# Optimization experiments

Hardware: AMD Instinct MI355X
Metric: run time of the kernel (lower is better)

The kernel has to match this reference:

```python
import jax, jax.numpy as jnp
import numpy as np

B, S, D = 4, 2048, 1024
N_NEURONS, K = 512, 8
N_BASIS, R = 32, 512
N_HEADS = 8
D_HEAD = R // N_HEADS


def setup_inputs() -> dict:
    key = jax.random.key(0)
    ks = jax.random.split(key, 8)
    x = jax.random.normal(ks[0], (B, S, D), dtype=jnp.float32)
    W_router = jax.random.normal(ks[1], (N_NEURONS, D), dtype=jnp.float32) / np.sqrt(D)
    recipe_Q = jax.random.normal(ks[2], (N_NEURONS, N_BASIS), dtype=jnp.float32)
    recipe_K = jax.random.normal(ks[3], (N_NEURONS, N_BASIS), dtype=jnp.float32)
    recipe_V = jax.random.normal(ks[4], (N_NEURONS, N_BASIS), dtype=jnp.float32)
    # orthonormal basis: QR of random [D, R] per basis slot (buffer, not trained)
    raw = jax.random.normal(ks[5], (N_BASIS, D, R), dtype=jnp.float32)
    basis = jax.vmap(lambda m: jnp.linalg.qr(m)[0])(raw)  # [N_BASIS, D, R]
    W_o = jax.random.normal(ks[6], (D, R), dtype=jnp.float32) / np.sqrt(R)
    mask = jnp.tril(jnp.ones((S, S), dtype=jnp.int32))[None, None]  # [1,1,S,S] causal
    mask = jnp.broadcast_to(mask, (B, 1, S, S))
    return {"x": x, "W_router": W_router, "recipe_Q": recipe_Q, "recipe_K": recipe_K,
            "recipe_V": recipe_V, "basis": basis, "W_o": W_o, "mask": mask}


def reference(x, W_router, recipe_Q, recipe_K, recipe_V, basis, W_o, mask):
    # routing: pick top-k neurons per token
    scores = jnp.einsum('bsd,nd->bsn', x, W_router)            # [B,S,N_NEURONS]
    topk_scores, topk_idx = jax.lax.top_k(scores, K)            # [B,S,K]
    weights = jax.nn.softmax(topk_scores, axis=-1)              # [B,S,K]

    def token_recipe(recipe):
        g = recipe[topk_idx]                                    # [B,S,K,N_BASIS]
        r = jnp.einsum('bskn,bsk->bsn', g, weights)             # [B,S,N_BASIS]
        return jax.nn.softmax(r, axis=-1)

    tQ = token_recipe(recipe_Q)
    tK = token_recipe(recipe_K)
    tV = token_recipe(recipe_V)

    # shared basis projection of x, reused for Q/K/V (same math as
    # W = einsum('bsn,ndr->bsdr'); Q = einsum('bsd,bsdr->bsr'))
    P = jnp.einsum('bsd,ndr->bsnr', x, basis)                   # [B,S,N_BASIS,R]
    Q = jnp.einsum('bsnr,bsn->bsr', P, tQ)
    Kt = jnp.einsum('bsnr,bsn->bsr', P, tK)
    V = jnp.einsum('bsnr,bsn->bsr', P, tV)

    def heads(t):
        return t.reshape(B, S, N_HEADS, D_HEAD).transpose(0, 2, 1, 3)  # [B,H,S,dh]

    Qh, Kh, Vh = heads(Q), heads(Kt), heads(V)
    attn = jnp.einsum('bhqd,bhkd->bhqk', Qh, Kh) / np.sqrt(D_HEAD)
    attn = jnp.where(mask == 0, jnp.float32(-1e30), attn)
    attn = jax.nn.softmax(attn, axis=-1)                        # dropout p: eval/no-op
    out = jnp.einsum('bhqk,bhkd->bhqd', attn, Vh)
    out = out.transpose(0, 2, 1, 3).reshape(B, S, R)
    attn_out = jnp.einsum('bsr,dr->bsd', out, W_o)
    return attn_out, topk_idx, weights
```

## Files before the change

kernel.cpp:

```cpp
#include <hip/hip_runtime.h>
#include <math.h>
#include <stdint.h>


typedef __attribute__((ext_vector_type(4))) float f32x4;
typedef __attribute__((ext_vector_type(8))) short s16x8;
typedef __attribute__((ext_vector_type(4))) short s16x4;
typedef __attribute__((ext_vector_type(4))) int i32x4;
typedef __attribute__((ext_vector_type(8))) int i32x8;

#define DEV __device__ __forceinline__

DEV short f2bf(float f){
  union { float f; unsigned u; } c; c.f = f;
  unsigned u = c.u;
  unsigned r = (u + 0x7fffu + ((u >> 16) & 1u)) >> 16;
  return (short)r;
}
DEV float bf2f(short s){
  union { unsigned u; float f; } c; c.u = ((unsigned)(unsigned short)s) << 16;
  return c.f;
}
DEV unsigned char f2e4m3(float f){
  union { float f; unsigned u; } c; c.f = f;
  unsigned u = c.u;
  unsigned sign = (u >> 24) & 0x80u;
  unsigned a = u & 0x7fffffffu;
  if (a >= 0x43e00000u) return (unsigned char)(sign | 0x7Eu);
  if (a < 0x3c800000u){
    union { unsigned u; float f; } d; d.u = a;
    int q = (int)(d.f * 512.0f + 0.5f);
    return (unsigned char)(sign | (unsigned)q);
  }
  unsigned m = a & 0x7fffffu;
  unsigned e = (a >> 23) - 120u;
  unsigned keep = m >> 20;
  unsigned rest = m & 0xFFFFFu;
  if (rest > 0x80000u || (rest == 0x80000u && (keep & 1u))){
    keep++;
    if (keep == 8u){ keep = 0; e++; }
  }
  if (e >= 16u || (e == 15u && keep == 7u)) return (unsigned char)(sign | 0x7Eu);
  return (unsigned char)(sign | (e << 3) | keep);
}

typedef __attribute__((address_space(3))) void lds_vt;
typedef const __attribute__((address_space(1))) void g_vt;
DEV void gload16(const void* g, void* lds){
  __builtin_amdgcn_global_load_lds((g_vt*)g, (lds_vt*)lds, 16, 0, 0);
}

DEV int gslot(int c){ return (c < 4) ? (c << 1) : (((c - 4) << 1) + 1); }

__global__ void k_conv_w(const float* __restrict__ Wo, const float* __restrict__ Wrt,
                         short* __restrict__ Wob, short* __restrict__ Wrtb){
  int i = blockIdx.x*256 + threadIdx.x;
  const float* src = (i < 131072) ? Wo : Wrt;
  short* dst = (i < 131072) ? Wob : Wrtb;
  int j = (i < 131072) ? i : (i - 131072);
  float4 v = ((const float4*)src)[j];
  s16x4 o; o[0]=f2bf(v.x); o[1]=f2bf(v.y); o[2]=f2bf(v.z); o[3]=f2bf(v.w);
  ((s16x4*)dst)[j] = o;
}

__global__ void k_conv_x(const float* __restrict__ in, short* __restrict__ Xb, char* __restrict__ Xf8){
  int t = blockIdx.x*256 + threadIdx.x;
  size_t d = (size_t)t * 16;
  const float4* s = (const float4*)(in + d);
  float vals[16];
  #pragma unroll
  for (int q=0;q<4;q++){ float4 v = s[q]; vals[q*4]=v.x; vals[q*4+1]=v.y; vals[q*4+2]=v.z; vals[q*4+3]=v.w; }
  s16x8 ob0, ob1;
  unsigned long long v0 = 0, v1 = 0;
  #pragma unroll
  for (int e=0;e<8;e++){
    ob0[e] = f2bf(vals[e]);
    ob1[e] = f2bf(vals[8+e]);
    v0 |= ((unsigned long long)f2e4m3(vals[e]))   << (8*e);
    v1 |= ((unsigned long long)f2e4m3(vals[8+e])) << (8*e);
  }
  *(s16x8*)(Xb + d) = ob0;
  *(s16x8*)(Xb + d + 8) = ob1;
  int c = t & 7;
  char* dst = Xf8 + (d & ~(size_t)127) + (gslot(c) << 4);
  *(unsigned long long*)dst = v0;
  *(unsigned long long*)(dst + 8) = v1;
}

__global__ __launch_bounds__(256) void k_conv_basis8(const float* __restrict__ basis, char* __restrict__ B2f){
  __shared__ float tile[64][65];
  int tid = threadIdx.x;
  int r0 = blockIdx.x<<6, d0 = blockIdx.y<<6, n = blockIdx.z;
  const float* src = basis + ((size_t)n*1024 + d0)*512 + r0;
  for (int i = tid; i < 4096; i += 256){ int dd = i>>6, rr = i&63; tile[dd][rr] = src[(size_t)dd*512 + rr]; }
  __syncthreads();
  int rr = tid >> 2, j = tid & 3;
  unsigned long long v0 = 0, v1 = 0;
  #pragma unroll
  for (int e=0;e<8;e++){
    v0 |= ((unsigned long long)f2e4m3(tile[j*16+e][rr]))   << (8*e);
    v1 |= ((unsigned long long)f2e4m3(tile[j*16+8+e][rr])) << (8*e);
  }
  int c = j + ((d0 >> 4) & 4);
  char* dst = B2f + ((size_t)(r0+rr)*32 + n)*1024 + (size_t)(d0 & ~127) + (gslot(c) << 4);
  *(unsigned long long*)dst = v0;
  *(unsigned long long*)(dst + 8) = v1;
}

__global__ __launch_bounds__(256) void k_gemm_c32(
    const short* __restrict__ A, const short* __restrict__ Bt, int Kd, int Mblk,
    float* __restrict__ C, int ldc)
{
  __shared__ char smem[32768];
  short* Asm = (short*)smem;
  short* Bsm = (short*)(smem + 16384);
  int tid = threadIdx.x, lane = tid & 63, w = tid >> 6;
  int wr = w >> 1, wc = w & 1;
  int nwg = gridDim.x, bid = blockIdx.x;
  int sid = (bid & 7) * (nwg >> 3) + (bid >> 3);
  int row0 = (sid % Mblk) << 7;
  int col0 = (sid / Mblk) << 7;
  f32x4 acc[4][4];
  #pragma unroll
  for (int m=0;m<4;m++)
    #pragma unroll
    for (int nf=0;nf<4;nf++)
      #pragma unroll
      for (int e=0;e<4;e++) acc[m][nf][e] = 0.f;
  int lr8 = lane >> 3;
  int lk_sw = (((lane & 7) ^ (lane >> 3)) << 3);
  for (int k0 = 0; k0 < Kd; k0 += 64){
    #pragma unroll
    for (int i=0;i<4;i++){
      int chunk = (w<<2) + i;
      int r = (chunk<<3) + lr8;
      gload16(A  + (size_t)(row0 + r)*Kd + k0 + lk_sw, smem + chunk*1024);
      gload16(Bt + (size_t)(col0 + r)*Kd + k0 + lk_sw, smem + 16384 + chunk*1024);
    }
    __syncthreads();
    #pragma unroll
    for (int kk=0; kk<2; kk++){
      int csw = (kk*32 + ((lane>>4)<<3)) ^ ((lane & 7) << 3);
      s16x8 af[4], bfr[4];
      #pragma unroll
      for (int m=0;m<4;m++)
        af[m] = *(const s16x8*)(Asm + ((wr*64 + m*16 + (lane&15))*64 + csw));
      #pragma unroll
      for (int nf=0;nf<4;nf++)
        bfr[nf] = *(const s16x8*)(Bsm + ((wc*64 + nf*16 + (lane&15))*64 + csw));
      #pragma unroll
      for (int m=0;m<4;m++)
        #pragma unroll
        for (int nf=0;nf<4;nf++)
          acc[m][nf] = __builtin_amdgcn_mfma_f32_16x16x32_bf16(af[m], bfr[nf], acc[m][nf], 0, 0, 0);
    }
    __syncthreads();
  }
  #pragma unroll
  for (int m=0;m<4;m++)
    #pragma unroll
    for (int nf=0;nf<4;nf++)
      #pragma unroll
      for (int e=0;e<4;e++){
        int tok = wr*64 + m*16 + ((lane>>4)<<2) + e;
        int col = wc*64 + nf*16 + (lane&15);
        C[(size_t)(row0+tok)*ldc + col0 + col] = acc[m][nf][e];
      }
}

#define STAGE_A(slotOff, arow0, tkt) do{ \
  int _t = (tkt) < 7 ? (tkt) : 7; \
  int _r = tid>>3, _g = tid&7; \
  gload16(B2f + (size_t)(row0 + (arow0) + _r)*1024 + (_t<<7) + ((_g ^ (_r&7))<<4), \
          smem + (slotOff) + (_r<<7) + (_g<<4)); \
}while(0)

#define STAGE_B(slotOff, trow0, tkt) do{ \
  int _t = (tkt) < 7 ? (tkt) : 7; \
  int _r = tid>>3, _g = tid&7; \
  gload16(Xf8 + (size_t)(col0 + (trow0) + _r)*1024 + (_t<<7) + ((_g ^ (_r&7))<<4), \
          smem + (slotOff) + (_r<<7) + (_g<<4)); \
  gload16(Xf8 + (size_t)(col0 + (trow0) + 64 + _r)*1024 + (_t<<7) + ((_g ^ (_r&7))<<4), \
          smem + (slotOff) + ((64+_r)<<7) + (_g<<4)); \
}while(0)

#define LD_AF(dst, base) \
  _Pragma("unroll") \
  for (int mi=0;mi<2;mi++){ \
    const char* _p = (base) + (wm*32 + mi*16 + l15)*128; \
    i32x4* _h = (i32x4*)&dst[mi]; \
    _h[0] = *(const i32x4*)(_p + ((ga0 ^ l7)<<4)); \
    _h[1] = *(const i32x4*)(_p + ((ga1 ^ l7)<<4)); \
  }

#define LD_BF(dst, base) \
  _Pragma("unroll") \
  for (int ni=0;ni<2;ni++){ \
    const char* _p = (base) + (wn*32 + ni*16 + l15)*128; \
    i32x4* _h = (i32x4*)&dst[ni]; \
    _h[0] = *(const i32x4*)(_p + ((ga0 ^ l7)<<4)); \
    _h[1] = *(const i32x4*)(_p + ((ga1 ^ l7)<<4)); \
  }

#define VMC(N) asm volatile("s_waitcnt vmcnt(" #N ")" ::: "memory")
#define PBAR() do{ __builtin_amdgcn_sched_barrier(0); __builtin_amdgcn_s_barrier(); }while(0)

#define MFMAP(Q, AF, BF) do{ \
  __builtin_amdgcn_s_setprio(1); \
  _Pragma("unroll") \
  for (int mi=0;mi<2;mi++) \
    _Pragma("unroll") \
    for (int ni=0;ni<2;ni++) \
      acc[Q][mi][ni] = __builtin_amdgcn_mfma_scale_f32_16x16x128_f8f6f4( \
          AF[mi], BF[ni], acc[Q][mi][ni], 0, 0, 0, 0x7f7f7f7f, 0, 0x7f7f7f7f); \
  __builtin_amdgcn_s_setprio(0); \
}while(0)

__global__ __launch_bounds__(512, 4) void k_pgemm8(
    const char* __restrict__ B2f, const char* __restrict__ Xf8,
    const float* __restrict__ tQp, const float* __restrict__ tKp, const float* __restrict__ tVp,
    short* __restrict__ Qb, short* __restrict__ Kb, short* __restrict__ Vt)
{
  extern __shared__ char smem[];
  int tid = threadIdx.x, lane = tid & 63, wid = tid >> 6;
  int wm = wid >> 2, wn = wid & 3;
  int l15 = lane & 15, l7 = lane & 7, g16 = lane >> 4;
  int ga0 = (g16 < 2) ? (g16 << 2) : (((g16 - 2) << 2) + 1);
  int ga1 = ga0 + 2;
  int bid = blockIdx.x;
  int xcd = bid & 7, lid = bid >> 3;
  int t_tile = (xcd << 2) + (lid & 3);
  int c_tile = lid >> 2;
  int row0 = c_tile << 7;
  int col0 = t_tile << 8;

  f32x4 acc[4][2][2];
  #pragma unroll
  for (int q=0;q<4;q++)
    #pragma unroll
    for (int mi=0;mi<2;mi++)
      #pragma unroll
      for (int ni=0;ni<2;ni++)
        #pragma unroll
        for (int e=0;e<4;e++) acc[q][mi][ni][e] = 0.f;
  i32x8 af[2], bf[2];

  STAGE_A(0, 0, 0);
  STAGE_B(24576, 0, 0);
  STAGE_A(16384, 64, 0);
  VMC(1);
  PBAR();

  for (int kt = 0; kt < 8; ++kt){
    const char* A0c = smem + ((kt&1)<<13);
    LD_AF(af, A0c);
    LD_BF(bf, smem + 24576);
    STAGE_B(40960, 128, kt);
    VMC(2);
    PBAR();
    MFMAP(0, af, bf);
    LD_AF(af, smem + 16384);
    STAGE_A(((kt+1)&1)<<13, 0, kt+1);
    VMC(1);
    PBAR();
    MFMAP(1, af, bf);
    LD_BF(bf, smem + 40960);
    STAGE_B(24576, 0, kt+1);
    PBAR();
    MFMAP(2, af, bf);
    LD_AF(af, A0c);
    STAGE_A(16384, 64, kt+1);
    VMC(1);
    PBAR();
    MFMAP(3, af, bf);
  }

  VMC(0);
  __syncthreads();
  short* t16 = (short*)smem;
  for (int i = tid; i < 8192; i += 512){
    int tk = i >> 5, n = i & 31;
    t16[tk*36 + n]            = f2bf(tQp[(size_t)col0*32 + i]);
    t16[9216 + tk*36 + n]     = f2bf(tKp[(size_t)col0*32 + i]);
    t16[18432 + tk*36 + n]    = f2bf(tVp[(size_t)col0*32 + i]);
  }
  __syncthreads();
  int g4 = g16 << 2;
  #pragma unroll
  for (int rec=0; rec<3; rec++){
    const short* tb = t16 + rec*9216;
    #pragma unroll
    for (int q=0;q<4;q++){
      int rh = (q==1)||(q==2);
      int ch = q >> 1;
      int r = (c_tile << 2) + rh*2 + wm;
      #pragma unroll
      for (int ni=0;ni<2;ni++){
        int tok = ch*128 + wn*32 + ni*16 + l15;
        s16x4 tlo = *(const s16x4*)(tb + tok*36 + g4);
        s16x4 thi = *(const s16x4*)(tb + tok*36 + 16 + g4);
        float p = 0.f;
        #pragma unroll
        for (int e=0;e<4;e++) p += acc[q][0][ni][e] * bf2f(tlo[e]);
        #pragma unroll
        for (int e=0;e<4;e++) p += acc[q][1][ni][e] * bf2f(thi[e]);
        p += __shfl_xor(p, 16);
        p += __shfl_xor(p, 32);
        if (g16 == rec){
          int gtok = col0 + tok;
          if (rec == 0)      Qb[(size_t)gtok*512 + r] = f2bf(p);
          else if (rec == 1) Kb[(size_t)gtok*512 + r] = f2bf(p);
          else Vt[(((size_t)(gtok>>11)*8 + (r>>6))*64 + (r&63))*2048 + (gtok&2047)] = f2bf(p);
        }
      }
    }
  }
}

__global__ __launch_bounds__(64) void k_router(const float* __restrict__ scores,
    const float* __restrict__ X, const float* __restrict__ W,
    const float* __restrict__ rQ, const float* __restrict__ rK, const float* __restrict__ rV,
    float* __restrict__ tQ, float* __restrict__ tK, float* __restrict__ tV,
    float* __restrict__ oidx, float* __restrict__ ow){
  int token = blockIdx.x; int lane = threadIdx.x;
  const float* srow = scores + (size_t)token*512;
  float v[8];
  #pragma unroll
  for (int j=0;j<8;j++) v[j] = srow[lane + 64*j];
  int myidx = 0x7fffffff;
  #pragma unroll
  for (int k=0;k<16;k++){
    float bm = -INFINITY; int bi = 0x7fffffff;
    #pragma unroll
    for (int j=0;j<8;j++){ if (v[j] > bm) { bm = v[j]; bi = lane + 64*j; } }
    #pragma unroll
    for (int off=32; off>=1; off>>=1){
      float om = __shfl_xor(bm, off); int oi = __shfl_xor(bi, off);
      if (om > bm || (om == bm && oi < bi)) { bm = om; bi = oi; }
    }
    if (lane == k) myidx = bi;
    #pragma unroll
    for (int j=0;j<8;j++) if (lane + 64*j == bi) v[j] = -INFINITY;
  }
  float xr[16];
  {
    const float4* x4 = (const float4*)(X + (size_t)token*1024 + lane*16);
    #pragma unroll
    for (int q=0;q<4;q++){ float4 t = x4[q]; xr[q*4]=t.x; xr[q*4+1]=t.y; xr[q*4+2]=t.z; xr[q*4+3]=t.w; }
  }
  double myref = -1e300;
  #pragma unroll
  for (int c=0;c<16;c++){
    int nid = __shfl(myidx, c);
    const float4* w4 = (const float4*)(W + (size_t)nid*1024 + lane*16);
    double acc = 0.0;
    #pragma unroll
    for (int q=0;q<4;q++){
      float4 t = w4[q];
      acc += (double)xr[q*4]   * (double)t.x;
      acc += (double)xr[q*4+1] * (double)t.y;
      acc += (double)xr[q*4+2] * (double)t.z;
      acc += (double)xr[q*4+3] * (double)t.w;
    }
    #pragma unroll
    for (int off=32; off>=1; off>>=1) acc += __shfl_xor(acc, off);
    if (lane == c) myref = acc;
  }
  double mv = myref; int mi = myidx;
  double topv[8]; int topi[8];
  #pragma unroll
  for (int k=0;k<8;k++){
    double bm = mv; int bi = mi;
    #pragma unroll
    for (int off=32; off>=1; off>>=1){
      double om = __shfl_xor(bm, off); int oi = __shfl_xor(bi, off);
      if (om > bm || (om == bm && oi < bi)) { bm = om; bi = oi; }
    }
    topv[k]=bm; topi[k]=bi;
    if (mi == bi) mv = -1e300;
  }
  double mx = topv[0]; double s = 0.0; double wd[8];
  #pragma unroll
  for (int k=0;k<8;k++){ wd[k] = exp(topv[k]-mx); s += wd[k]; }
  float w[8];
  #pragma unroll
  for (int k=0;k<8;k++) w[k] = (float)(wd[k]/s);
  if (lane == 0){
    #pragma unroll
    for (int k=0;k<8;k++){ oidx[(size_t)token*8+k] = (float)topi[k]; ow[(size_t)token*8+k] = w[k]; }
  }
  int n = lane & 31;
  float aq=0.f, ak=0.f, av=0.f;
  #pragma unroll
  for (int k=0;k<8;k++){
    size_t off = (size_t)topi[k]*32 + n;
    aq += w[k]*rQ[off]; ak += w[k]*rK[off]; av += w[k]*rV[off];
  }
  float mq = aq, mk2 = ak, mvv = av;
  #pragma unroll
  for (int off=16; off>=1; off>>=1){
    mq  = fmaxf(mq,  __shfl_xor(mq, off));
    mk2 = fmaxf(mk2, __shfl_xor(mk2,off));
    mvv = fmaxf(mvv, __shfl_xor(mvv,off));
  }
  float eq = expf(aq-mq), ek = expf(ak-mk2), ev = expf(av-mvv);
  float sq = eq, sk = ek, sv = ev;
  #pragma unroll
  for (int off=16; off>=1; off>>=1){
    sq += __shfl_xor(sq,off); sk += __shfl_xor(sk,off); sv += __shfl_xor(sv,off);
  }
  if (lane < 32){
    tQ[(size_t)token*32+n] = eq/sq;
    tK[(size_t)token*32+n] = ek/sk;
    tV[(size_t)token*32+n] = ev/sv;
  }
}

__global__ __launch_bounds__(256) void k_attn(const short* __restrict__ Qb, const short* __restrict__ Kb,
                                              const short* __restrict__ Vt, short* __restrict__ Ob)
{
  __shared__ char smem[40960];
  int tid = threadIdx.x, lane = tid & 63, wid = tid >> 6;
  int l15 = lane & 15, l7 = lane & 7, g16 = lane >> 4;
  int bid = blockIdx.x;
  int xcd = bid & 7, lid = bid >> 3;
  int work = xcd*128 + lid;
  int bx = 31 - (work & 31);
  int bh = work >> 5; int h = bh & 7, b = bh >> 3;
  size_t tokbase = (size_t)b*2048;
  int q0 = bx << 6;
  int nt = bx + 1;
  const float SC = 0.125f * 1.44269504f;

#define ATTN_STAGE(kt_) do{ \
  int _c = (kt_) & 1; \
  _Pragma("unroll") \
  for (int _i=0;_i<2;_i++){ \
    int _row = _i*32 + (wid<<3) + (lane>>3); \
    gload16(Kb + (tokbase + (((kt_)<<6) + _row))*512 + (h<<6) + ((l7 ^ (_row&7))<<3), \
            smem + (_c<<13) + _i*4096 + (wid<<10) + lane*16); \
    gload16(Vt + (size_t)((bh<<6) + _row)*2048 + ((kt_)<<6) + ((l7 ^ (_row&7))<<3), \
            smem + 16384 + (_c<<13) + _i*4096 + (wid<<10) + lane*16); \
  } \
}while(0)

  s16x8 qf[2];
  {
    const short* qp = Qb + (tokbase + q0 + wid*16 + l15)*512 + (h<<6);
    qf[0] = *(const s16x8*)(qp + g16*8);
    qf[1] = *(const s16x8*)(qp + 32 + g16*8);
  }
  int q_abs = q0 + wid*16 + l15;
  f32x4 o[4];
  float m_log = -INFINITY, l_sum = 0.f;
  #pragma unroll
  for (int i=0;i<4;i++)
    #pragma unroll
    for (int e=0;e<4;e++) o[i][e]=0.f;

  ATTN_STAGE(0);
  __syncthreads();

  for (int kt = 0; kt < nt; ++kt){
    if (kt + 1 < nt) ATTN_STAGE(kt+1);
    int cur = kt & 1;
    const char* Kc = smem + (cur<<13);
    const char* Vc = smem + 16384 + (cur<<13);
    char* Pb = smem + 32768 + (wid<<11);
    f32x4 S[4];
    #pragma unroll
    for (int s16=0;s16<4;s16++){
      #pragma unroll
      for (int e=0;e<4;e++) S[s16][e] = 0.f;
      const char* kr = Kc + (s16*16 + l15)*128;
      s16x8 kf0 = *(const s16x8*)(kr + (((g16  ) ^ l7)<<4));
      s16x8 kf1 = *(const s16x8*)(kr + (((4+g16) ^ l7)<<4));
      S[s16] = __builtin_amdgcn_mfma_f32_16x16x32_bf16(kf0, qf[0], S[s16], 0,0,0);
      S[s16] = __builtin_amdgcn_mfma_f32_16x16x32_bf16(kf1, qf[1], S[s16], 0,0,0);
    }
    bool diag = (kt == nt-1);
    float sm[16];
    #pragma unroll
    for (int s16=0;s16<4;s16++)
      #pragma unroll
      for (int e=0;e<4;e++){
        float sv = S[s16][e] * SC;
        if (diag){
          int kv_abs = (kt<<6) + s16*16 + (g16<<2) + e;
          if (kv_abs > q_abs) sv = -1e30f;
        }
        sm[s16*4+e] = sv;
      }
    float pmax = sm[0];
    #pragma unroll
    for (int j=1;j<16;j++) pmax = fmaxf(pmax, sm[j]);
    pmax = fmaxf(pmax, __shfl_xor(pmax, 16));
    pmax = fmaxf(pmax, __shfl_xor(pmax, 32));
    float mnew = fmaxf(m_log, pmax);
    float alpha = exp2f(m_log - mnew);
    m_log = mnew;
    float p[16], ps = 0.f;
    #pragma unroll
    for (int j=0;j<16;j++){ p[j] = exp2f(sm[j] - mnew); ps += p[j]; }
    ps += __shfl_xor(ps, 16);
    ps += __shfl_xor(ps, 32);
    l_sum = l_sum*alpha + ps;
    #pragma unroll
    for (int e=0;e<4;e++){
      float al = __shfl(alpha, (g16<<2)+e);
      #pragma unroll
      for (int df=0;df<4;df++) o[df][e] *= al;
    }
    #pragma unroll
    for (int s16=0;s16<4;s16++){
      s16x4 pk;
      #pragma unroll
      for (int e=0;e<4;e++) pk[e] = f2bf(p[s16*4+e]);
      *(s16x4*)(Pb + l15*128 + (((s16<<5) + (g16<<3)) ^ (l7<<4))) = pk;
    }
    s16x8 pf0 = *(const s16x8*)(Pb + l15*128 + (((g16  ) ^ l7)<<4));
    s16x8 pf1 = *(const s16x8*)(Pb + l15*128 + (((4+g16) ^ l7)<<4));
    #pragma unroll
    for (int df=0;df<4;df++){
      const char* vr = Vc + (df*16 + l15)*128;
      s16x8 vf0 = *(const s16x8*)(vr + (((g16  ) ^ l7)<<4));
      s16x8 vf1 = *(const s16x8*)(vr + (((4+g16) ^ l7)<<4));
      o[df] = __builtin_amdgcn_mfma_f32_16x16x32_bf16(pf0, vf0, o[df], 0,0,0);
      o[df] = __builtin_amdgcn_mfma_f32_16x16x32_bf16(pf1, vf1, o[df], 0,0,0);
    }
    __syncthreads();
  }
  #pragma unroll
  for (int e=0;e<4;e++){
    float ln = __shfl(l_sum, (g16<<2)+e);
    float inv = 1.0f / ln;
    #pragma unroll
    for (int df=0;df<4;df++){
      int q = q0 + wid*16 + (g16<<2) + e;
      int d = df*16 + l15;
      Ob[(tokbase + q)*512 + (h<<6) + d] = f2bf(o[df][e] * inv);
    }
  }
#undef ATTN_STAGE
}

extern "C" void kernel_launch(void* const* d_in, const int* in_sizes, int n_in,
                              void* d_out, int out_size, void* d_ws, size_t ws_size,
                              hipStream_t stream)
{
  const float* x     = (const float*)d_in[0];
  const float* Wrt   = (const float*)d_in[1];
  const float* rQ    = (const float*)d_in[2];
  const float* rK    = (const float*)d_in[3];
  const float* rV    = (const float*)d_in[4];
  const float* basis = (const float*)d_in[5];
  const float* Wo    = (const float*)d_in[6];
  float* out = (float*)d_out;
  char* ws = (char*)d_ws;
  char*  B2f  = (char*)(ws + 0);
  char*  Xf8  = (char*)(ws + 16777216);
  short* Xb   = (short*)(ws + 25165824);
  float* SC   = (float*)(ws + 41943040);
  float* tQ   = (float*)(ws + 58720256);
  float* tK   = (float*)(ws + 59768832);
  float* tV   = (float*)(ws + 60817408);
  short* Qb   = (short*)(ws + 61865984);
  short* Kb   = (short*)(ws + 70254592);
  short* Vt   = (short*)(ws + 78643200);
  short* Ob   = (short*)(ws + 87031808);
  short* Wob  = (short*)(ws + 95420416);
  short* Wrtb = (short*)(ws + 96468992);
  float* oidx = out + 8388608;
  float* oww  = out + 8454144;

  hipFuncSetAttribute((const void*)k_pgemm8, hipFuncAttributeMaxDynamicSharedMemorySize, 57344);

  k_conv_x<<<2048, 256, 0, stream>>>(x, Xb, Xf8);
  k_conv_w<<<1024, 256, 0, stream>>>(Wo, Wrt, Wob, Wrtb);
  k_conv_basis8<<<dim3(8,16,32), 256, 0, stream>>>(basis, B2f);
  k_gemm_c32<<<256, 256, 0, stream>>>(Xb, Wrtb, 1024, 64, SC, 512);
  k_router<<<8192, 64, 0, stream>>>(SC, x, Wrt, rQ, rK, rV, tQ, tK, tV, oidx, oww);
  k_pgemm8<<<4096, 512, 57344, stream>>>(B2f, Xf8, tQ, tK, tV, Qb, Kb, Vt);
  k_attn<<<1024, 256, 0, stream>>>(Qb, Kb, Vt, Ob);
  k_gemm_c32<<<512, 256, 0, stream>>>(Ob, Wob, 512, 64, out, 1024);
}
```

Baseline: 399.8 us.

## Load K/V attention fragments directly from global memory, drop LDS staging

The attention kernel no longer stages K and V tiles into shared memory through a double-buffered async copy. Each wave now reads its MFMA fragments straight from global memory, relying on L1/L2 because all four waves read the same K/V rows. Only the per-wave P buffer stays in LDS, which removes the block-wide barrier per tile and cuts LDS use, so more blocks can fit per CU. The cost is redundant global loads across waves and no explicit prefetch, so latency may be exposed.

```diff
diff --git a/kernel.cpp b/kernel.cpp
--- a/kernel.cpp
+++ b/kernel.cpp
@@ -419,7 +419,7 @@
 __global__ __launch_bounds__(256) void k_attn(const short* __restrict__ Qb, const short* __restrict__ Kb,
                                               const short* __restrict__ Vt, short* __restrict__ Ob)
 {
-  __shared__ char smem[40960];
+  __shared__ char smem[8192];
   int tid = threadIdx.x, lane = tid & 63, wid = tid >> 6;
   int l15 = lane & 15, l7 = lane & 7, g16 = lane >> 4;
   int bid = blockIdx.x;
@@ -432,18 +432,6 @@
   int nt = bx + 1;
   const float SC = 0.125f * 1.44269504f;
 
-#define ATTN_STAGE(kt_) do{ \
-  int _c = (kt_) & 1; \
-  _Pragma("unroll") \
-  for (int _i=0;_i<2;_i++){ \
-    int _row = _i*32 + (wid<<3) + (lane>>3); \
-    gload16(Kb + (tokbase + (((kt_)<<6) + _row))*512 + (h<<6) + ((l7 ^ (_row&7))<<3), \
-            smem + (_c<<13) + _i*4096 + (wid<<10) + lane*16); \
-    gload16(Vt + (size_t)((bh<<6) + _row)*2048 + ((kt_)<<6) + ((l7 ^ (_row&7))<<3), \
-            smem + 16384 + (_c<<13) + _i*4096 + (wid<<10) + lane*16); \
-  } \
-}while(0)
-
   s16x8 qf[2];
   {
     const short* qp = Qb + (tokbase + q0 + wid*16 + l15)*512 + (h<<6);
@@ -458,23 +446,20 @@
     #pragma unroll
     for (int e=0;e<4;e++) o[i][e]=0.f;
 
-  ATTN_STAGE(0);
-  __syncthreads();
+  char* Pb = smem + (wid<<11);
+  const short* Krow0 = Kb + tokbase*512 + (h<<6);
+  const short* Vrow0 = Vt + ((size_t)(bh<<6))*2048;
 
   for (int kt = 0; kt < nt; ++kt){
-    if (kt + 1 < nt) ATTN_STAGE(kt+1);
-    int cur = kt & 1;
-    const char* Kc = smem + (cur<<13);
-    const char* Vc = smem + 16384 + (cur<<13);
-    char* Pb = smem + 32768 + (wid<<11);
+    int kv0 = kt << 6;
     f32x4 S[4];
     #pragma unroll
     for (int s16=0;s16<4;s16++){
       #pragma unroll
       for (int e=0;e<4;e++) S[s16][e] = 0.f;
-      const char* kr = Kc + (s16*16 + l15)*128;
-      s16x8 kf0 = *(const s16x8*)(kr + (((g16  ) ^ l7)<<4));
-      s16x8 kf1 = *(const s16x8*)(kr + (((4+g16) ^ l7)<<4));
+      const short* kr = Krow0 + (size_t)(kv0 + s16*16 + l15)*512 + g16*8;
+      s16x8 kf0 = *(const s16x8*)(kr);
+      s16x8 kf1 = *(const s16x8*)(kr + 32);
       S[s16] = __builtin_amdgcn_mfma_f32_16x16x32_bf16(kf0, qf[0], S[s16], 0,0,0);
       S[s16] = __builtin_amdgcn_mfma_f32_16x16x32_bf16(kf1, qf[1], S[s16], 0,0,0);
     }
@@ -486,7 +471,7 @@
       for (int e=0;e<4;e++){
         float sv = S[s16][e] * SC;
         if (diag){
-          int kv_abs = (kt<<6) + s16*16 + (g16<<2) + e;
+          int kv_abs = kv0 + s16*16 + (g16<<2) + e;
           if (kv_abs > q_abs) sv = -1e30f;
         }
         sm[s16*4+e] = sv;
@@ -511,6 +496,8 @@
       #pragma unroll
       for (int df=0;df<4;df++) o[df][e] *= al;
     }
+    asm volatile("s_waitcnt lgkmcnt(0)" ::: "memory");
+    __builtin_amdgcn_sched_barrier(0);
     #pragma unroll
     for (int s16=0;s16<4;s16++){
       s16x4 pk;
@@ -518,17 +505,18 @@
       for (int e=0;e<4;e++) pk[e] = f2bf(p[s16*4+e]);
       *(s16x4*)(Pb + l15*128 + (((s16<<5) + (g16<<3)) ^ (l7<<4))) = pk;
     }
+    asm volatile("s_waitcnt lgkmcnt(0)" ::: "memory");
+    __builtin_amdgcn_sched_barrier(0);
     s16x8 pf0 = *(const s16x8*)(Pb + l15*128 + (((g16  ) ^ l7)<<4));
     s16x8 pf1 = *(const s16x8*)(Pb + l15*128 + (((4+g16) ^ l7)<<4));
     #pragma unroll
     for (int df=0;df<4;df++){
-      const char* vr = Vc + (df*16 + l15)*128;
-      s16x8 vf0 = *(const s16x8*)(vr + (((g16  ) ^ l7)<<4));
-      s16x8 vf1 = *(const s16x8*)(vr + (((4+g16) ^ l7)<<4));
+      const short* vr = Vrow0 + (size_t)(df*16 + l15)*2048 + kv0 + g16*8;
+      s16x8 vf0 = *(const s16x8*)(vr);
+      s16x8 vf1 = *(const s16x8*)(vr + 32);
       o[df] = __builtin_amdgcn_mfma_f32_16x16x32_bf16(pf0, vf0, o[df], 0,0,0);
       o[df] = __builtin_amdgcn_mfma_f32_16x16x32_bf16(pf1, vf1, o[df], 0,0,0);
     }
-    __syncthreads();
   }
   #pragma unroll
   for (int e=0;e<4;e++){
@@ -541,7 +529,6 @@
       Ob[(tokbase + q)*512 + (h<<6) + d] = f2bf(o[df][e] * inv);
     }
   }
-#undef ATTN_STAGE
 }
 
 extern "C" void kernel_launch(void* const* d_in, const int* in_sizes, int n_in,
```

Result: slower. 531.4 us (+32.9%).
